# Kernel optimization log

Measured on AMD Instinct MI355X. Metric: run time of the kernel, lower is better.

Reference implementation:

```python
import jax, jax.numpy as jnp
import numpy as np

B = 4096
INPUT = 1024
HIDDEN = 2048
D_INNER = 2 * HIDDEN      # expand=2
DT_RANK = HIDDEN // 16    # 128
D_STATE = 16
LN_EPS = 1e-5


def setup_inputs() -> dict:
    key = jax.random.key(0)
    ks = jax.random.split(key, 12)
    s = lambda fan_in: 1.0 / np.sqrt(fan_in)
    inp = {
        "x": jax.random.normal(ks[0], (B, INPUT), jnp.float32),
        "h": jax.random.normal(ks[1], (B, HIDDEN), jnp.float32),
        # in_proj: Linear(input_size, 2*d_inner, bias=False)
        "W_in": jax.random.uniform(ks[2], (2 * D_INNER, INPUT), jnp.float32, -s(INPUT), s(INPUT)),
        # state_proj: Linear(hidden, d_inner, bias=False)
        "W_state": jax.random.uniform(ks[3], (D_INNER, HIDDEN), jnp.float32, -s(HIDDEN), s(HIDDEN)),
        # x_proj: Linear(d_inner, dt_rank + 2*d_state, bias=False)
        "W_xproj": jax.random.uniform(ks[4], (DT_RANK + 2 * D_STATE, D_INNER), jnp.float32, -s(D_INNER), s(D_INNER)),
        # dt_proj: Linear(dt_rank, d_inner, bias=True), weight ~ U(-dt_rank^-0.5, dt_rank^-0.5)
        "W_dt": jax.random.uniform(ks[5], (D_INNER, DT_RANK), jnp.float32, -s(DT_RANK), s(DT_RANK)),
        "b_dt": jnp.log(jnp.expm1(jnp.exp(jax.random.uniform(ks[6], (D_INNER,), jnp.float32)
                                           * (np.log(0.1) - np.log(0.001)) + np.log(0.001)))),
        # A_log = log(arange(1, d_state+1)) repeated over d_inner (unused in single-step math)
        "A_log": jnp.broadcast_to(jnp.log(jnp.arange(1, D_STATE + 1, dtype=jnp.float32)), (D_INNER, D_STATE)),
        "D": jnp.ones((D_INNER,), jnp.float32),
        # out_proj: Linear(d_inner, hidden, bias=False)
        "W_out": jax.random.uniform(ks[7], (HIDDEN, D_INNER), jnp.float32, -s(D_INNER), s(D_INNER)),
        # LayerNorm(hidden)
        "gamma": jnp.ones((HIDDEN,), jnp.float32),
        "beta": jnp.zeros((HIDDEN,), jnp.float32),
    }
    return inp


def _layernorm(x, gamma, beta):
    mu = jnp.mean(x, axis=-1, keepdims=True)
    var = jnp.mean(jnp.square(x - mu), axis=-1, keepdims=True)
    return (x - mu) * jax.lax.rsqrt(var + LN_EPS) * gamma + beta


def reference(x, h, W_in, W_state, W_xproj, W_dt, b_dt, A_log, D, W_out, gamma, beta):
    # in_proj and split into x branch / gate z
    xz = x @ W_in.T                               # [B, 2*d_inner]
    x_br, z = jnp.split(xz, 2, axis=-1)
    # add projected previous hidden state, then SiLU
    x_br = jax.nn.silu(x_br + h @ W_state.T)      # [B, d_inner]
    # x_proj -> (dt, B_mat, C)
    x_dbl = x_br @ W_xproj.T                      # [B, dt_rank + 2*d_state]
    dt_lo = x_dbl[:, :DT_RANK]
    B_mat = x_dbl[:, DT_RANK:DT_RANK + D_STATE]   # [B, d_state]
    C_mat = x_dbl[:, DT_RANK + D_STATE:]          # [B, d_state]
    dt = jax.nn.softplus(dt_lo @ W_dt.T + b_dt)   # [B, d_inner]
    # ssm_out[b,d] = sum_n dt[b,d]*B[b,n]*x_br[b,d]*C[b,n] + D[d]*x_br[b,d]
    bc = jnp.sum(B_mat * C_mat, axis=-1, keepdims=True)  # [B, 1]
    ssm_out = dt * x_br * bc + D * x_br           # [B, d_inner]
    # gate, output projection, residual, layernorm
    y = ssm_out * jax.nn.silu(z)
    h_new = y @ W_out.T + h
    return _layernorm(h_new, gamma, beta)
```

## Files before the change

### kernel.cpp

```cpp
#include <hip/hip_runtime.h>
#include <hip/hip_bf16.h>
#include <cstdint>
#include <cstddef>

typedef unsigned short u16;
typedef __bf16 bf16x8 __attribute__((ext_vector_type(8)));
typedef float f32x4 __attribute__((ext_vector_type(4)));
typedef float f32x16 __attribute__((ext_vector_type(16)));

#define B_ROWS 4096
#define N_HIDDEN 2048
#define DT_RANK 128

static __device__ __forceinline__ u16 f2bf(float f) {
  unsigned u = __float_as_uint(f);
  u += 0x7FFFu + ((u >> 16) & 1u);
  return (u16)(u >> 16);
}
static __device__ __forceinline__ float bf2f(u16 b) {
  return __uint_as_float(((unsigned)b) << 16);
}
static __device__ __forceinline__ float siluf(float v) {
  return v / (1.0f + __expf(-v));
}
static __device__ __forceinline__ float softplusf(float v) {
  return v > 15.0f ? v : log1pf(__expf(v));
}
static __device__ __forceinline__ void async16(void* lds, const void* g) {
  __builtin_amdgcn_global_load_lds((const __attribute__((address_space(1))) void*)g,
                                   (__attribute__((address_space(3))) void*)lds, 16, 0, 0);
}

__global__ void cvt_bf16_kernel(const float* __restrict__ in, u16* __restrict__ out, int n4) {
  int i = blockIdx.x * blockDim.x + threadIdx.x;
  const int stride = gridDim.x * blockDim.x;
  for (; i < n4; i += stride) {
    float4 f = ((const float4*)in)[i];
    ushort4 o;
    o.x = f2bf(f.x); o.y = f2bf(f.y); o.z = f2bf(f.z); o.w = f2bf(f.w);
    ((ushort4*)out)[i] = o;
  }
}

__global__ void cvt_rows_kernel(const float* __restrict__ src, u16* __restrict__ dst,
                                int rl4, int dstride) {
  const int row = blockIdx.x;
  const float4* s = (const float4*)(src + (size_t)row * (rl4 * 4));
  ushort4* d = (ushort4*)(dst + (size_t)row * dstride);
  for (int c = threadIdx.x; c < rl4; c += blockDim.x) {
    float4 f = s[c];
    ushort4 o;
    o.x = f2bf(f.x); o.y = f2bf(f.y); o.z = f2bf(f.z); o.w = f2bf(f.w);
    d[c] = o;
  }
}

template <int NN, int KK, int LDA, int LDB, int EPI>
__global__ __launch_bounds__(512, 1)
void gemm8(const u16* __restrict__ A, const u16* __restrict__ Bw,
           float* __restrict__ outf, u16* __restrict__ outb, long long zstride)
{
  extern __shared__ u16 lds[];
  u16* ldsA = lds;
  u16* ldsB = lds + 32768;
  constexpr int NT = KK / 64;
  static_assert(NT >= 3, "schedule assumes NT >= 3");

  const int t = threadIdx.x;
  const int lane = t & 63, w = t >> 6;
  const int wr = w >> 2, wc = w & 3;
  const int r32 = lane & 31;
  const int kg = lane >> 5;

  const int gx = gridDim.x;
  const int nwg = gx * gridDim.y;
  const int bid = blockIdx.y * gx + blockIdx.x;
  const int cpx = nwg >> 3;
  const int swz = (bid & 7) * cpx + (bid >> 3);
  const int n0 = (swz % gx) * 256;
  const int m0 = (swz / gx) * 256;
  const int koff = blockIdx.z * KK;

  f32x16 acc[4][2] = {};

  auto stA = [&](int buf, int half, int k0) {
#pragma unroll
    for (int i = 0; i < 2; ++i) {
      const int ii = w * 2 + i;
      const int c = ii * 64 + lane;
      const int row = c >> 3;
      const int ch = (c & 7) ^ (row & 7);
      async16(ldsA + (buf * 2 + half) * 8192 + ii * 512,
              A + (size_t)(m0 + half * 128 + row) * LDA + (koff + k0 + ch * 8));
    }
  };
  auto stB = [&](int buf, int half, int k0) {
#pragma unroll
    for (int i = 0; i < 2; ++i) {
      const int ii = w * 2 + i;
      const int c = ii * 64 + lane;
      const int row = c >> 3;
      const int ch = (c & 7) ^ (row & 7);
      async16(ldsB + (buf * 2 + half) * 8192 + ii * 512,
              Bw + (size_t)(n0 + half * 128 + row) * LDB + (koff + k0 + ch * 8));
    }
  };

  const int aSlotHalf = wr;
  const int bSlotHalf = wc >> 1;
  const int lrB0 = (wc & 1) * 64;

  auto ldA = [&](int buf, int lr, int ks) -> bf16x8 {
    const int tt = ks * 2 + kg;
    return *(const bf16x8*)(ldsA + (size_t)((buf * 2 + aSlotHalf) * 8192 + lr * 64 + ((tt ^ (lr & 7)) << 3)));
  };
  auto ldB = [&](int buf, int lr, int ks) -> bf16x8 {
    const int tt = ks * 2 + kg;
    return *(const bf16x8*)(ldsB + (size_t)((buf * 2 + bSlotHalf) * 8192 + lr * 64 + ((tt ^ (lr & 7)) << 3)));
  };

  stA(0, 0, 0); stA(0, 1, 0); stB(0, 0, 0); stB(0, 1, 0);
  stA(1, 0, 64);
  asm volatile("s_waitcnt vmcnt(2)" ::: "memory");
  __builtin_amdgcn_s_barrier();
  asm volatile("" ::: "memory");

  int cur = 0;
  for (int j = 0; j < NT; ++j) {
    const int nxt = cur ^ 1;
    bf16x8 af0[4], af1[4], af2[4], af3[4], bb0[2], bb1[2], bb2[2], bb3[2];
#pragma unroll
    for (int fi = 0; fi < 4; ++fi) af0[fi] = ldA(cur, fi * 32 + r32, 0);
#pragma unroll
    for (int g = 0; g < 2; ++g) { bb0[g] = ldB(cur, lrB0 + g * 32 + r32, 0); bb1[g] = ldB(cur, lrB0 + g * 32 + r32, 1); }
    if (j + 1 < NT) stA(nxt, 1, (j + 1) * 64);
    asm volatile("" ::: "memory");
    __builtin_amdgcn_s_barrier();
    asm volatile("s_waitcnt lgkmcnt(0)" ::: "memory");
    __builtin_amdgcn_s_setprio(1);
#pragma unroll
    for (int fi = 0; fi < 4; ++fi)
#pragma unroll
      for (int g = 0; g < 2; ++g)
        acc[fi][g] = __builtin_amdgcn_mfma_f32_32x32x16_bf16(af0[fi], bb0[g], acc[fi][g], 0, 0, 0);
    __builtin_amdgcn_s_setprio(0);
    asm volatile("" ::: "memory");
    __builtin_amdgcn_s_barrier();
    asm volatile("" ::: "memory");
#pragma unroll
    for (int fi = 0; fi < 4; ++fi) af1[fi] = ldA(cur, fi * 32 + r32, 1);
#pragma unroll
    for (int g = 0; g < 2; ++g) { bb2[g] = ldB(cur, lrB0 + g * 32 + r32, 2); bb3[g] = ldB(cur, lrB0 + g * 32 + r32, 3); }
    if (j + 1 < NT) stB(nxt, 0, (j + 1) * 64);
    asm volatile("" ::: "memory");
    __builtin_amdgcn_s_barrier();
    asm volatile("s_waitcnt lgkmcnt(0)" ::: "memory");
    __builtin_amdgcn_s_setprio(1);
#pragma unroll
    for (int fi = 0; fi < 4; ++fi)
#pragma unroll
      for (int g = 0; g < 2; ++g)
        acc[fi][g] = __builtin_amdgcn_mfma_f32_32x32x16_bf16(af1[fi], bb1[g], acc[fi][g], 0, 0, 0);
    __builtin_amdgcn_s_setprio(0);
    asm volatile("" ::: "memory");
    __builtin_amdgcn_s_barrier();
    asm volatile("" ::: "memory");
#pragma unroll
    for (int fi = 0; fi < 4; ++fi) af2[fi] = ldA(cur, fi * 32 + r32, 2);
#pragma unroll
    for (int fi = 0; fi < 4; ++fi) af3[fi] = ldA(cur, fi * 32 + r32, 3);
    if (j + 1 < NT) stB(nxt, 1, (j + 1) * 64);
    asm volatile("" ::: "memory");
    __builtin_amdgcn_s_barrier();
    asm volatile("s_waitcnt lgkmcnt(0)" ::: "memory");
    __builtin_amdgcn_s_setprio(1);
#pragma unroll
    for (int fi = 0; fi < 4; ++fi)
#pragma unroll
      for (int g = 0; g < 2; ++g)
        acc[fi][g] = __builtin_amdgcn_mfma_f32_32x32x16_bf16(af2[fi], bb2[g], acc[fi][g], 0, 0, 0);
    __builtin_amdgcn_s_setprio(0);
    asm volatile("" ::: "memory");
    __builtin_amdgcn_s_barrier();
    asm volatile("" ::: "memory");
    if (j + 2 < NT) stA(cur, 0, (j + 2) * 64);
    asm volatile("" ::: "memory");
    __builtin_amdgcn_s_barrier();
    __builtin_amdgcn_s_setprio(1);
#pragma unroll
    for (int fi = 0; fi < 4; ++fi)
#pragma unroll
      for (int g = 0; g < 2; ++g)
        acc[fi][g] = __builtin_amdgcn_mfma_f32_32x32x16_bf16(af3[fi], bb3[g], acc[fi][g], 0, 0, 0);
    __builtin_amdgcn_s_setprio(0);
    if (j + 2 < NT) { asm volatile("s_waitcnt vmcnt(2)" ::: "memory"); }
    else            { asm volatile("s_waitcnt vmcnt(0)" ::: "memory"); }
    asm volatile("" ::: "memory");
    __builtin_amdgcn_s_barrier();
    asm volatile("" ::: "memory");
    cur = nxt;
  }

  float* of = outf ? (outf + (size_t)blockIdx.z * zstride) : nullptr;
#pragma unroll
  for (int fi = 0; fi < 4; ++fi) {
#pragma unroll
    for (int g = 0; g < 2; ++g) {
#pragma unroll
      for (int reg = 0; reg < 16; ++reg) {
        const int grow = m0 + wr * 128 + fi * 32 + (reg & 3) + 8 * (reg >> 2) + 4 * kg;
        const int gcol = n0 + wc * 64 + g * 32 + r32;
        const float v = acc[fi][g][reg];
        if constexpr (EPI == 0) {
          outb[(size_t)grow * NN + gcol] = f2bf(siluf(v));
        } else {
          of[(size_t)grow * NN + gcol] = v;
        }
      }
    }
  }
}

template <int NN, int KK, int LDA, int EPI>
__global__ __launch_bounds__(256)
void gemm_bt(const u16* __restrict__ A, const u16* __restrict__ Bw,
             float* __restrict__ outf, u16* __restrict__ outb,
             const float* __restrict__ aux1, const float* __restrict__ aux2,
             const float* __restrict__ aux3,
             const u16* __restrict__ xaux, const u16* __restrict__ saux)
{
  constexpr int BM = 128, BK = 64;
  __shared__ alignas(16) u16 As[2][BM * BK];
  __shared__ alignas(16) u16 Bs[2][BM * BK];
  const int t = threadIdx.x;
  const int lane = t & 63, w = t >> 6;
  const int m0 = blockIdx.y * BM, n0 = blockIdx.x * BM;
  const int mw = (w >> 1) * 64, nw = (w & 1) * 64;
  const int r = lane & 15;
  const int kq = (lane >> 4) * 8;

  f32x4 acc[4][4] = {};

  auto stage = [&](int buf, int k0) {
#pragma unroll
    for (int i = 0; i < 4; ++i) {
      const int slot0 = (w * 4 + i) * 64;
      const int s = slot0 + lane;
      const int row = s >> 3, cs = (s & 7) * 8;
      async16(&As[buf][slot0 * 8], A + (size_t)(m0 + row) * LDA + k0 + cs);
      async16(&Bs[buf][slot0 * 8], Bw + (size_t)(n0 + row) * KK + k0 + cs);
    }
  };

  stage(0, 0);
  asm volatile("s_waitcnt vmcnt(0)" ::: "memory");
  __syncthreads();
  int cur = 0;

  for (int k0 = 0; k0 < KK; k0 += BK) {
    if (k0 + BK < KK) stage(cur ^ 1, k0 + BK);
#pragma unroll
    for (int kk = 0; kk < BK; kk += 32) {
      bf16x8 af[4], bb[4];
#pragma unroll
      for (int f = 0; f < 4; ++f)
        af[f] = *(const bf16x8*)(&As[cur][(mw + f * 16 + r) * BK + kk + kq]);
#pragma unroll
      for (int f = 0; f < 4; ++f)
        bb[f] = *(const bf16x8*)(&Bs[cur][(nw + f * 16 + r) * BK + kk + kq]);
#pragma unroll
      for (int fm = 0; fm < 4; ++fm)
#pragma unroll
        for (int fn = 0; fn < 4; ++fn)
          acc[fm][fn] = __builtin_amdgcn_mfma_f32_16x16x32_bf16(af[fm], bb[fn], acc[fm][fn], 0, 0, 0);
    }
    asm volatile("s_waitcnt vmcnt(0)" ::: "memory");
    __syncthreads();
    cur ^= 1;
  }

  const int rr = (lane >> 4) * 4;
  const int cc = lane & 15;
#pragma unroll
  for (int fm = 0; fm < 4; ++fm) {
#pragma unroll
    for (int fn = 0; fn < 4; ++fn) {
#pragma unroll
      for (int tt = 0; tt < 4; ++tt) {
        const int grow = m0 + mw + fm * 16 + rr + tt;
        const int gcol = n0 + nw + fn * 16 + cc;
        float v = acc[fm][fn][tt];
        if constexpr (EPI == 2) {
          float dt = softplusf(v + aux1[gcol]);
          float xv = bf2f(xaux[(size_t)grow * NN + gcol]);
          float sv = bf2f(saux[(size_t)grow * NN + gcol]);
          float yv = xv * (dt * aux2[grow] + aux3[gcol]) * sv;
          outb[(size_t)grow * NN + gcol] = f2bf(yv);
        } else {
          outf[(size_t)grow * NN + gcol] = v;
        }
      }
    }
  }
}

__global__ __launch_bounds__(256)
void gemm_xproj(const u16* __restrict__ A, const u16* __restrict__ Bw,
                float* __restrict__ part)
{
  constexpr int BK = 64;
  __shared__ alignas(16) u16 As[64 * BK];
  __shared__ alignas(16) u16 Bs[160 * BK];
  const int t = threadIdx.x, lane = t & 63, w = t >> 6;
  const int m0 = blockIdx.x * 64;
  const int kz = blockIdx.y;
  const int r = lane & 15, kq = (lane >> 4) * 8;
  f32x4 acc[10] = {};
  for (int kt = 0; kt < 1024; kt += BK) {
    const int k0 = kz * 1024 + kt;
#pragma unroll
    for (int i = 0; i < 2; ++i) {
      const int slot0 = (w * 2 + i) * 64;
      const int s = slot0 + lane;
      async16(As + slot0 * 8, A + (size_t)(m0 + (s >> 3)) * 4096 + k0 + (s & 7) * 8);
    }
#pragma unroll
    for (int i = 0; i < 5; ++i) {
      const int slot0 = (w * 5 + i) * 64;
      const int s = slot0 + lane;
      async16(Bs + slot0 * 8, Bw + (size_t)(s >> 3) * 4096 + k0 + (s & 7) * 8);
    }
    asm volatile("s_waitcnt vmcnt(0)" ::: "memory");
    __syncthreads();
#pragma unroll
    for (int kk = 0; kk < BK; kk += 32) {
      bf16x8 af = *(const bf16x8*)(As + (w * 16 + r) * BK + kk + kq);
#pragma unroll
      for (int fn = 0; fn < 10; ++fn) {
        bf16x8 bb = *(const bf16x8*)(Bs + (fn * 16 + r) * BK + kk + kq);
        acc[fn] = __builtin_amdgcn_mfma_f32_16x16x32_bf16(af, bb, acc[fn], 0, 0, 0);
      }
    }
    __syncthreads();
  }
  float* o = part + (size_t)kz * B_ROWS * 160;
  const int rr = (lane >> 4) * 4, cc = lane & 15;
#pragma unroll
  for (int fn = 0; fn < 10; ++fn)
#pragma unroll
    for (int tt = 0; tt < 4; ++tt)
      o[(size_t)(m0 + w * 16 + rr + tt) * 160 + fn * 16 + cc] = acc[fn][tt];
}

__global__ __launch_bounds__(192)
void xdbl_reduce(const float* __restrict__ part, u16* __restrict__ dtlo,
                 float* __restrict__ bc)
{
  const int row = blockIdx.x, t = threadIdx.x;
  __shared__ float cvals[32];
  float v = 0.0f;
  if (t < 160) {
    const float* p = part + (size_t)row * 160 + t;
#pragma unroll
    for (int z = 0; z < 4; ++z) v += p[(size_t)z * B_ROWS * 160];
  }
  if (t < DT_RANK) dtlo[(size_t)row * DT_RANK + t] = f2bf(v);
  if (t >= DT_RANK && t < 160) cvals[t - DT_RANK] = v;
  __syncthreads();
  if (t == 0) {
    float s = 0.0f;
#pragma unroll
    for (int j = 0; j < 16; ++j) s += cvals[j] * cvals[j + 16];
    bc[row] = s;
  }
}

__global__ __launch_bounds__(256)
void ln_kernel(const float* __restrict__ p0, const float* __restrict__ p1,
               const float* __restrict__ hh, const float* __restrict__ gamma,
               const float* __restrict__ beta, float* __restrict__ out)
{
  const int row = blockIdx.x, t = threadIdx.x;
  __shared__ float red[4];
  const float4* x0 = (const float4*)(p0 + (size_t)row * N_HIDDEN);
  const float4* x1 = (const float4*)(p1 + (size_t)row * N_HIDDEN);
  const float4* xh = (const float4*)(hh + (size_t)row * N_HIDDEN);
  float4 a, b;
  {
    float4 u = x0[t], v = x1[t], w = xh[t];
    a.x = u.x + v.x + w.x; a.y = u.y + v.y + w.y; a.z = u.z + v.z + w.z; a.w = u.w + v.w + w.w;
    u = x0[t + 256]; v = x1[t + 256]; w = xh[t + 256];
    b.x = u.x + v.x + w.x; b.y = u.y + v.y + w.y; b.z = u.z + v.z + w.z; b.w = u.w + v.w + w.w;
  }
  float s = ((a.x + a.y) + (a.z + a.w)) + ((b.x + b.y) + (b.z + b.w));
#pragma unroll
  for (int m = 32; m; m >>= 1) s += __shfl_xor(s, m);
  if ((t & 63) == 0) red[t >> 6] = s;
  __syncthreads();
  s = (red[0] + red[1]) + (red[2] + red[3]);
  const float mu = s * (1.0f / N_HIDDEN);
  float dx0 = a.x - mu, dx1 = a.y - mu, dx2 = a.z - mu, dx3 = a.w - mu;
  float dy0 = b.x - mu, dy1 = b.y - mu, dy2 = b.z - mu, dy3 = b.w - mu;
  float q = ((dx0 * dx0 + dx1 * dx1) + (dx2 * dx2 + dx3 * dx3)) +
            ((dy0 * dy0 + dy1 * dy1) + (dy2 * dy2 + dy3 * dy3));
  __syncthreads();
#pragma unroll
  for (int m = 32; m; m >>= 1) q += __shfl_xor(q, m);
  if ((t & 63) == 0) red[t >> 6] = q;
  __syncthreads();
  q = (red[0] + red[1]) + (red[2] + red[3]);
  const float inv = rsqrtf(q * (1.0f / N_HIDDEN) + 1e-5f);
  const float4 ga = ((const float4*)gamma)[t], gb = ((const float4*)gamma)[t + 256];
  const float4 ba = ((const float4*)beta)[t], bbv = ((const float4*)beta)[t + 256];
  float4 o0, o1;
  o0.x = dx0 * inv * ga.x + ba.x;
  o0.y = dx1 * inv * ga.y + ba.y;
  o0.z = dx2 * inv * ga.z + ba.z;
  o0.w = dx3 * inv * ga.w + ba.w;
  o1.x = dy0 * inv * gb.x + bbv.x;
  o1.y = dy1 * inv * gb.y + bbv.y;
  o1.z = dy2 * inv * gb.z + bbv.z;
  o1.w = dy3 * inv * gb.w + bbv.w;
  float4* o4 = (float4*)(out + (size_t)row * N_HIDDEN);
  o4[t] = o0;
  o4[t + 256] = o1;
}

extern "C" void kernel_launch(void* const* d_in, const int* in_sizes, int n_in,
                              void* d_out, int out_size, void* d_ws, size_t ws_size,
                              hipStream_t stream) {
  const float* x     = (const float*)d_in[0];
  const float* h     = (const float*)d_in[1];
  const float* W_in  = (const float*)d_in[2];
  const float* W_st  = (const float*)d_in[3];
  const float* W_xp  = (const float*)d_in[4];
  const float* W_dt  = (const float*)d_in[5];
  const float* b_dt  = (const float*)d_in[6];
  const float* Dv    = (const float*)d_in[8];
  const float* W_out = (const float*)d_in[9];
  const float* gamma = (const float*)d_in[10];
  const float* beta  = (const float*)d_in[11];
  float* out = (float*)d_out;
  (void)in_sizes; (void)n_in; (void)out_size; (void)ws_size;

  char* ws = (char*)d_ws;
  size_t o = 0;
  auto alloc = [&](size_t bytes) { char* p = ws + o; o += bytes; return p; };
  u16* Acat    = (u16*)alloc((size_t)4096 * 3072 * 2);
  u16* Wcat    = (u16*)alloc((size_t)4096 * 3072 * 2);
  u16* Wz_bf   = (u16*)alloc((size_t)4096 * 1024 * 2);
  u16* Wxp_bf  = (u16*)alloc((size_t)160 * 4096 * 2);
  u16* Wdt_bf  = (u16*)alloc((size_t)4096 * 128 * 2);
  u16* Wout_bf = (u16*)alloc((size_t)2048 * 4096 * 2);
  u16* xbr_bf  = (u16*)alloc((size_t)4096 * 4096 * 2);
  u16* sz_bf   = (u16*)alloc((size_t)4096 * 4096 * 2);
  float* part  = (float*)alloc((size_t)4 * 4096 * 160 * 4);
  u16* dtlo_bf = (u16*)alloc((size_t)4096 * 128 * 2);
  float* bc    = (float*)alloc((size_t)4096 * 4);
  u16* y_bf = (u16*)Acat;
  float* p0 = (float*)xbr_bf;
  float* p1 = p0 + (size_t)4096 * 2048;

  auto cvt = [&](const float* src, u16* dst, size_t n) {
    int n4 = (int)(n / 4);
    int blocks = (n4 + 255) / 256;
    if (blocks > 2048) blocks = 2048;
    cvt_bf16_kernel<<<blocks, 256, 0, stream>>>(src, dst, n4);
  };
  cvt_rows_kernel<<<4096, 256, 0, stream>>>(x,    Acat,        256, 3072);
  cvt_rows_kernel<<<4096, 256, 0, stream>>>(h,    Acat + 1024, 512, 3072);
  cvt_rows_kernel<<<4096, 256, 0, stream>>>(W_in, Wcat,        256, 3072);
  cvt_rows_kernel<<<4096, 256, 0, stream>>>(W_st, Wcat + 1024, 512, 3072);
  cvt(W_in + (size_t)4096 * 1024, Wz_bf, (size_t)4096 * 1024);
  cvt(W_xp, Wxp_bf, (size_t)160 * 4096);
  cvt(W_dt, Wdt_bf, (size_t)4096 * 128);
  cvt(W_out, Wout_bf, (size_t)2048 * 4096);

  gemm8<4096, 3072, 3072, 3072, 0><<<dim3(16, 16, 1), 512, 131072, stream>>>(
      Acat, Wcat, nullptr, xbr_bf, 0);
  gemm8<4096, 1024, 3072, 1024, 0><<<dim3(16, 16, 1), 512, 131072, stream>>>(
      Acat, Wz_bf, nullptr, sz_bf, 0);
  gemm_xproj<<<dim3(64, 4), 256, 0, stream>>>(xbr_bf, Wxp_bf, part);
  xdbl_reduce<<<4096, 192, 0, stream>>>(part, dtlo_bf, bc);
  gemm_bt<4096, 128, 128, 2><<<dim3(32, 32), 256, 0, stream>>>(
      dtlo_bf, Wdt_bf, nullptr, y_bf, b_dt, bc, Dv, xbr_bf, sz_bf);
  gemm8<2048, 2048, 4096, 4096, 1><<<dim3(8, 16, 2), 512, 131072, stream>>>(
      y_bf, Wout_bf, p0, nullptr, (long long)4096 * 2048);
  ln_kernel<<<4096, 256, 0, stream>>>(p0, p1, h, gamma, beta, out);
}
```

Baseline: 399.4 us.

## Switch GEMM to 16x16x32 MFMA quadrant schedule and merge conversion launches

```diff
diff --git a/kernel.cpp b/kernel.cpp
--- a/kernel.cpp
+++ b/kernel.cpp
@@ -6,7 +6,6 @@
 typedef unsigned short u16;
 typedef __bf16 bf16x8 __attribute__((ext_vector_type(8)));
 typedef float f32x4 __attribute__((ext_vector_type(4)));
-typedef float f32x16 __attribute__((ext_vector_type(16)));
 
 #define B_ROWS 4096
 #define N_HIDDEN 2048
@@ -31,22 +30,23 @@
                                    (__attribute__((address_space(3))) void*)lds, 16, 0, 0);
 }
 
-__global__ void cvt_bf16_kernel(const float* __restrict__ in, u16* __restrict__ out, int n4) {
-  int i = blockIdx.x * blockDim.x + threadIdx.x;
-  const int stride = gridDim.x * blockDim.x;
-  for (; i < n4; i += stride) {
-    float4 f = ((const float4*)in)[i];
-    ushort4 o;
-    o.x = f2bf(f.x); o.y = f2bf(f.y); o.z = f2bf(f.z); o.w = f2bf(f.w);
-    ((ushort4*)out)[i] = o;
-  }
-}
-
-__global__ void cvt_rows_kernel(const float* __restrict__ src, u16* __restrict__ dst,
-                                int rl4, int dstride) {
-  const int row = blockIdx.x;
-  const float4* s = (const float4*)(src + (size_t)row * (rl4 * 4));
-  ushort4* d = (ushort4*)(dst + (size_t)row * dstride);
+struct CvtJobs {
+  const float* src[8];
+  u16* dst[8];
+  int rl4[8];
+  int dstride[8];
+  int cum[9];
+};
+__global__ __launch_bounds__(256)
+void cvt_all_kernel(CvtJobs J) {
+  int b = blockIdx.x;
+  int job = 0;
+#pragma unroll
+  for (int k = 1; k < 8; ++k) if (b >= J.cum[k]) job = k;
+  const int row = b - J.cum[job];
+  const int rl4 = J.rl4[job];
+  const float4* s = (const float4*)(J.src[job] + (size_t)row * (rl4 * 4));
+  ushort4* d = (ushort4*)(J.dst[job] + (size_t)row * J.dstride[job]);
   for (int c = threadIdx.x; c < rl4; c += blockDim.x) {
     float4 f = s[c];
     ushort4 o;
@@ -64,13 +64,13 @@
   u16* ldsA = lds;
   u16* ldsB = lds + 32768;
   constexpr int NT = KK / 64;
-  static_assert(NT >= 3, "schedule assumes NT >= 3");
+  static_assert(NT >= 2, "schedule assumes NT >= 2");
 
   const int t = threadIdx.x;
   const int lane = t & 63, w = t >> 6;
   const int wr = w >> 2, wc = w & 3;
-  const int r32 = lane & 31;
-  const int kg = lane >> 5;
+  const int r = lane & 15;
+  const int q4 = lane >> 4;
 
   const int gx = gridDim.x;
   const int nwg = gx * gridDim.y;
@@ -81,7 +81,7 @@
   const int m0 = (swz / gx) * 256;
   const int koff = blockIdx.z * KK;
 
-  f32x16 acc[4][2] = {};
+  f32x4 acc[2][2][4][2] = {};
 
   auto stA = [&](int buf, int half, int k0) {
 #pragma unroll
@@ -106,34 +106,37 @@
     }
   };
 
-  const int aSlotHalf = wr;
-  const int bSlotHalf = wc >> 1;
-  const int lrB0 = (wc & 1) * 64;
-
-  auto ldA = [&](int buf, int lr, int ks) -> bf16x8 {
-    const int tt = ks * 2 + kg;
-    return *(const bf16x8*)(ldsA + (size_t)((buf * 2 + aSlotHalf) * 8192 + lr * 64 + ((tt ^ (lr & 7)) << 3)));
+  auto ldA = [&](int buf, int half, int lr, int kki) -> bf16x8 {
+    const int tt = kki * 4 + q4;
+    return *(const bf16x8*)(ldsA + (size_t)((buf * 2 + half) * 8192 + lr * 64 + ((tt ^ (lr & 7)) << 3)));
   };
-  auto ldB = [&](int buf, int lr, int ks) -> bf16x8 {
-    const int tt = ks * 2 + kg;
-    return *(const bf16x8*)(ldsB + (size_t)((buf * 2 + bSlotHalf) * 8192 + lr * 64 + ((tt ^ (lr & 7)) << 3)));
+  auto ldB = [&](int buf, int half, int lr, int kki) -> bf16x8 {
+    const int tt = kki * 4 + q4;
+    return *(const bf16x8*)(ldsB + (size_t)((buf * 2 + half) * 8192 + lr * 64 + ((tt ^ (lr & 7)) << 3)));
   };
 
-  stA(0, 0, 0); stA(0, 1, 0); stB(0, 0, 0); stB(0, 1, 0);
-  stA(1, 0, 64);
-  asm volatile("s_waitcnt vmcnt(2)" ::: "memory");
+  stA(0, 0, 0); stB(0, 0, 0); stB(0, 1, 0); stA(0, 1, 0);
+  asm volatile("s_waitcnt vmcnt(4)" ::: "memory");
   __builtin_amdgcn_s_barrier();
   asm volatile("" ::: "memory");
 
   int cur = 0;
   for (int j = 0; j < NT; ++j) {
     const int nxt = cur ^ 1;
-    bf16x8 af0[4], af1[4], af2[4], af3[4], bb0[2], bb1[2], bb2[2], bb3[2];
-#pragma unroll
-    for (int fi = 0; fi < 4; ++fi) af0[fi] = ldA(cur, fi * 32 + r32, 0);
-#pragma unroll
-    for (int g = 0; g < 2; ++g) { bb0[g] = ldB(cur, lrB0 + g * 32 + r32, 0); bb1[g] = ldB(cur, lrB0 + g * 32 + r32, 1); }
-    if (j + 1 < NT) stA(nxt, 1, (j + 1) * 64);
+    const bool lastj = (j == NT - 1);
+    bf16x8 fa[8], fah[8], fb0[4], fb1[4];
+
+#pragma unroll
+    for (int fi = 0; fi < 4; ++fi)
+#pragma unroll
+      for (int ks = 0; ks < 2; ++ks)
+        fa[fi * 2 + ks] = ldA(cur, 0, wr * 64 + fi * 16 + r, ks);
+#pragma unroll
+    for (int g = 0; g < 2; ++g)
+#pragma unroll
+      for (int ks = 0; ks < 2; ++ks)
+        fb0[g * 2 + ks] = ldB(cur, 0, wc * 32 + g * 16 + r, ks);
+    if (j + 1 < NT) stA(nxt, 0, (j + 1) * 64);
     asm volatile("" ::: "memory");
     __builtin_amdgcn_s_barrier();
     asm volatile("s_waitcnt lgkmcnt(0)" ::: "memory");
@@ -141,16 +144,21 @@
 #pragma unroll
     for (int fi = 0; fi < 4; ++fi)
 #pragma unroll
-      for (int g = 0; g < 2; ++g)
-        acc[fi][g] = __builtin_amdgcn_mfma_f32_32x32x16_bf16(af0[fi], bb0[g], acc[fi][g], 0, 0, 0);
+      for (int g = 0; g < 2; ++g) {
+        acc[0][0][fi][g] = __builtin_amdgcn_mfma_f32_16x16x32_bf16(fa[fi * 2 + 0], fb0[g * 2 + 0], acc[0][0][fi][g], 0, 0, 0);
+        acc[0][0][fi][g] = __builtin_amdgcn_mfma_f32_16x16x32_bf16(fa[fi * 2 + 1], fb0[g * 2 + 1], acc[0][0][fi][g], 0, 0, 0);
+      }
     __builtin_amdgcn_s_setprio(0);
-    asm volatile("" ::: "memory");
-    __builtin_amdgcn_s_barrier();
-    asm volatile("" ::: "memory");
-#pragma unroll
-    for (int fi = 0; fi < 4; ++fi) af1[fi] = ldA(cur, fi * 32 + r32, 1);
-#pragma unroll
-    for (int g = 0; g < 2; ++g) { bb2[g] = ldB(cur, lrB0 + g * 32 + r32, 2); bb3[g] = ldB(cur, lrB0 + g * 32 + r32, 3); }
+    if (lastj) { asm volatile("s_waitcnt vmcnt(2)" ::: "memory"); }
+    else       { asm volatile("s_waitcnt vmcnt(4)" ::: "memory"); }
+    __builtin_amdgcn_s_barrier();
+    asm volatile("" ::: "memory");
+
+#pragma unroll
+    for (int g = 0; g < 2; ++g)
+#pragma unroll
+      for (int ks = 0; ks < 2; ++ks)
+        fb1[g * 2 + ks] = ldB(cur, 1, wc * 32 + g * 16 + r, ks);
     if (j + 1 < NT) stB(nxt, 0, (j + 1) * 64);
     asm volatile("" ::: "memory");
     __builtin_amdgcn_s_barrier();
@@ -159,16 +167,21 @@
 #pragma unroll
     for (int fi = 0; fi < 4; ++fi)
 #pragma unroll
-      for (int g = 0; g < 2; ++g)
-        acc[fi][g] = __builtin_amdgcn_mfma_f32_32x32x16_bf16(af1[fi], bb1[g], acc[fi][g], 0, 0, 0);
+      for (int g = 0; g < 2; ++g) {
+        acc[0][1][fi][g] = __builtin_amdgcn_mfma_f32_16x16x32_bf16(fa[fi * 2 + 0], fb1[g * 2 + 0], acc[0][1][fi][g], 0, 0, 0);
+        acc[0][1][fi][g] = __builtin_amdgcn_mfma_f32_16x16x32_bf16(fa[fi * 2 + 1], fb1[g * 2 + 1], acc[0][1][fi][g], 0, 0, 0);
+      }
     __builtin_amdgcn_s_setprio(0);
-    asm volatile("" ::: "memory");
-    __builtin_amdgcn_s_barrier();
-    asm volatile("" ::: "memory");
-#pragma unroll
-    for (int fi = 0; fi < 4; ++fi) af2[fi] = ldA(cur, fi * 32 + r32, 2);
-#pragma unroll
-    for (int fi = 0; fi < 4; ++fi) af3[fi] = ldA(cur, fi * 32 + r32, 3);
+    if (lastj) { asm volatile("s_waitcnt vmcnt(0)" ::: "memory"); }
+    else       { asm volatile("s_waitcnt vmcnt(4)" ::: "memory"); }
+    __builtin_amdgcn_s_barrier();
+    asm volatile("" ::: "memory");
+
+#pragma unroll
+    for (int fi = 0; fi < 4; ++fi)
+#pragma unroll
+      for (int ks = 0; ks < 2; ++ks)
+        fah[fi * 2 + ks] = ldA(cur, 1, wr * 64 + fi * 16 + r, ks);
     if (j + 1 < NT) stB(nxt, 1, (j + 1) * 64);
     asm volatile("" ::: "memory");
     __builtin_amdgcn_s_barrier();
@@ -177,24 +190,28 @@
 #pragma unroll
     for (int fi = 0; fi < 4; ++fi)
 #pragma unroll
-      for (int g = 0; g < 2; ++g)
-        acc[fi][g] = __builtin_amdgcn_mfma_f32_32x32x16_bf16(af2[fi], bb2[g], acc[fi][g], 0, 0, 0);
+      for (int g = 0; g < 2; ++g) {
+        acc[1][0][fi][g] = __builtin_amdgcn_mfma_f32_16x16x32_bf16(fah[fi * 2 + 0], fb0[g * 2 + 0], acc[1][0][fi][g], 0, 0, 0);
+        acc[1][0][fi][g] = __builtin_amdgcn_mfma_f32_16x16x32_bf16(fah[fi * 2 + 1], fb0[g * 2 + 1], acc[1][0][fi][g], 0, 0, 0);
+      }
     __builtin_amdgcn_s_setprio(0);
     asm volatile("" ::: "memory");
     __builtin_amdgcn_s_barrier();
     asm volatile("" ::: "memory");
-    if (j + 2 < NT) stA(cur, 0, (j + 2) * 64);
+
+    if (j + 1 < NT) stA(nxt, 1, (j + 1) * 64);
     asm volatile("" ::: "memory");
     __builtin_amdgcn_s_barrier();
     __builtin_amdgcn_s_setprio(1);
 #pragma unroll
     for (int fi = 0; fi < 4; ++fi)
 #pragma unroll
-      for (int g = 0; g < 2; ++g)
-        acc[fi][g] = __builtin_amdgcn_mfma_f32_32x32x16_bf16(af3[fi], bb3[g], acc[fi][g], 0, 0, 0);
+      for (int g = 0; g < 2; ++g) {
+        acc[1][1][fi][g] = __builtin_amdgcn_mfma_f32_16x16x32_bf16(fah[fi * 2 + 0], fb1[g * 2 + 0], acc[1][1][fi][g], 0, 0, 0);
+        acc[1][1][fi][g] = __builtin_amdgcn_mfma_f32_16x16x32_bf16(fah[fi * 2 + 1], fb1[g * 2 + 1], acc[1][1][fi][g], 0, 0, 0);
+      }
     __builtin_amdgcn_s_setprio(0);
-    if (j + 2 < NT) { asm volatile("s_waitcnt vmcnt(2)" ::: "memory"); }
-    else            { asm volatile("s_waitcnt vmcnt(0)" ::: "memory"); }
+    if (j + 1 < NT) { asm volatile("s_waitcnt vmcnt(4)" ::: "memory"); }
     asm volatile("" ::: "memory");
     __builtin_amdgcn_s_barrier();
     asm volatile("" ::: "memory");
@@ -203,22 +220,24 @@
 
   float* of = outf ? (outf + (size_t)blockIdx.z * zstride) : nullptr;
 #pragma unroll
-  for (int fi = 0; fi < 4; ++fi) {
-#pragma unroll
-    for (int g = 0; g < 2; ++g) {
-#pragma unroll
-      for (int reg = 0; reg < 16; ++reg) {
-        const int grow = m0 + wr * 128 + fi * 32 + (reg & 3) + 8 * (reg >> 2) + 4 * kg;
-        const int gcol = n0 + wc * 64 + g * 32 + r32;
-        const float v = acc[fi][g][reg];
-        if constexpr (EPI == 0) {
-          outb[(size_t)grow * NN + gcol] = f2bf(siluf(v));
-        } else {
-          of[(size_t)grow * NN + gcol] = v;
-        }
-      }
-    }
-  }
+  for (int a = 0; a < 2; ++a)
+#pragma unroll
+    for (int b = 0; b < 2; ++b)
+#pragma unroll
+      for (int fi = 0; fi < 4; ++fi)
+#pragma unroll
+        for (int g = 0; g < 2; ++g)
+#pragma unroll
+          for (int tt = 0; tt < 4; ++tt) {
+            const int grow = m0 + a * 128 + wr * 64 + fi * 16 + q4 * 4 + tt;
+            const int gcol = n0 + b * 128 + wc * 32 + g * 16 + r;
+            const float v = acc[a][b][fi][g][tt];
+            if constexpr (EPI == 0) {
+              outb[(size_t)grow * NN + gcol] = f2bf(siluf(v));
+            } else {
+              of[(size_t)grow * NN + gcol] = v;
+            }
+          }
 }
 
 template <int NN, int KK, int LDA, int EPI>
@@ -461,20 +480,19 @@
   float* p0 = (float*)xbr_bf;
   float* p1 = p0 + (size_t)4096 * 2048;
 
-  auto cvt = [&](const float* src, u16* dst, size_t n) {
-    int n4 = (int)(n / 4);
-    int blocks = (n4 + 255) / 256;
-    if (blocks > 2048) blocks = 2048;
-    cvt_bf16_kernel<<<blocks, 256, 0, stream>>>(src, dst, n4);
-  };
-  cvt_rows_kernel<<<4096, 256, 0, stream>>>(x,    Acat,        256, 3072);
-  cvt_rows_kernel<<<4096, 256, 0, stream>>>(h,    Acat + 1024, 512, 3072);
-  cvt_rows_kernel<<<4096, 256, 0, stream>>>(W_in, Wcat,        256, 3072);
-  cvt_rows_kernel<<<4096, 256, 0, stream>>>(W_st, Wcat + 1024, 512, 3072);
-  cvt(W_in + (size_t)4096 * 1024, Wz_bf, (size_t)4096 * 1024);
-  cvt(W_xp, Wxp_bf, (size_t)160 * 4096);
-  cvt(W_dt, Wdt_bf, (size_t)4096 * 128);
-  cvt(W_out, Wout_bf, (size_t)2048 * 4096);
+  CvtJobs J;
+  J.src[0] = x;                           J.dst[0] = Acat;        J.rl4[0] = 256;  J.dstride[0] = 3072;
+  J.src[1] = h;                           J.dst[1] = Acat + 1024; J.rl4[1] = 512;  J.dstride[1] = 3072;
+  J.src[2] = W_in;                        J.dst[2] = Wcat;        J.rl4[2] = 256;  J.dstride[2] = 3072;
+  J.src[3] = W_st;                        J.dst[3] = Wcat + 1024; J.rl4[3] = 512;  J.dstride[3] = 3072;
+  J.src[4] = W_in + (size_t)4096 * 1024;  J.dst[4] = Wz_bf;       J.rl4[4] = 256;  J.dstride[4] = 1024;
+  J.src[5] = W_xp;                        J.dst[5] = Wxp_bf;      J.rl4[5] = 1024; J.dstride[5] = 4096;
+  J.src[6] = W_dt;                        J.dst[6] = Wdt_bf;      J.rl4[6] = 32;   J.dstride[6] = 128;
+  J.src[7] = W_out;                       J.dst[7] = Wout_bf;     J.rl4[7] = 1024; J.dstride[7] = 4096;
+  const int rows[8] = {4096, 4096, 4096, 4096, 4096, 160, 4096, 2048};
+  J.cum[0] = 0;
+  for (int k = 0; k < 8; ++k) J.cum[k + 1] = J.cum[k] + rows[k];
+  cvt_all_kernel<<<J.cum[8], 256, 0, stream>>>(J);
 
   gemm8<4096, 3072, 3072, 3072, 0><<<dim3(16, 16, 1), 512, 131072, stream>>>(
       Acat, Wcat, nullptr, xbr_bf, 0);
```

Result: faster. 360.4 us (-9.8%).
